# Kernel optimization log

Hardware: AMD Instinct MI355X
Metric: run time of the kernel (lower is better)

## Reference

```python
import jax, jax.numpy as jnp
import numpy as np

N, E, C = 25000, 400000, 64
NUM_ELEM, NUM_BESSEL, HID, NPATH, L = 4, 8, 64, 5, 2
R_MAX, AVG_NN = 5.0, 16.0
SQRT3, SQRT2 = 3.0 ** 0.5, 2.0 ** 0.5


def setup_inputs() -> dict:
    key = jax.random.key(0)
    ks = jax.random.split(key, 16)
    def w(k, shape, fan_in):
        return jax.random.normal(k, shape, jnp.float32) / np.float32(np.sqrt(fan_in))
    return {
        "positions": jax.random.normal(ks[0], (N, 3), jnp.float32),
        "species": jax.random.randint(ks[1], (N,), 0, NUM_ELEM, jnp.int32),
        "edge_index": jax.random.randint(ks[2], (2, E), 0, N, jnp.int32),
        "node_embed_W": w(ks[3], (NUM_ELEM, C), NUM_ELEM),
        "lin_up_W0": w(ks[4], (L, C, C), C),
        "lin_up_W1": w(ks[5], (L, C, C), C),
        "mlp_W1": w(ks[6], (L, NUM_BESSEL, HID), NUM_BESSEL),
        "mlp_W2": w(ks[7], (L, HID, HID), HID),
        "mlp_W3": w(ks[8], (L, HID, NPATH * C), HID),
        "lin_W0": w(ks[9], (L, C, C), C),
        "lin_W1": w(ks[10], (L, C, C), C),
        "prod_W0": w(ks[11], (L, NUM_ELEM, 3, C), 3),
        "prod_W1": w(ks[12], (L, NUM_ELEM, 2, C), 2),
        "prod_lin_W0": w(ks[13], (L, C, C), C),
        "prod_lin_W1": w(ks[14], (L, C, C), C),
    }


def _poly_cutoff(r):  # MACE polynomial cutoff, p=6
    p = 6.0
    x = r / R_MAX
    f = (1.0 - 0.5 * (p + 1.0) * (p + 2.0) * x ** 6
         + p * (p + 2.0) * x ** 7 - 0.5 * p * (p + 1.0) * x ** 8)
    return f * (x < 1.0)


def reference(positions, species, edge_index, node_embed_W,
              lin_up_W0, lin_up_W1, mlp_W1, mlp_W2, mlp_W3,
              lin_W0, lin_W1, prod_W0, prod_W1, prod_lin_W0, prod_lin_W1):
    sender, receiver = edge_index[0], edge_index[1]
    vec = positions[sender] - positions[receiver]                  # [E,3]
    r = jnp.maximum(jnp.linalg.norm(vec, axis=-1), 1e-6)           # [E]
    u = vec / r[:, None]
    Y1 = SQRT3 * u                                                 # l=1 SH (component norm); Y0 == 1
    # Bessel radial embedding with polynomial cutoff -> edge_feats [E, NUM_BESSEL]
    n = jnp.arange(1, NUM_BESSEL + 1, dtype=jnp.float32)
    bessel = jnp.sqrt(2.0 / R_MAX) * jnp.sin(n[None, :] * jnp.pi * r[:, None] / R_MAX) / r[:, None]
    edge_feats = bessel * _poly_cutoff(r)[:, None]
    node_attrs = jax.nn.one_hot(species, NUM_ELEM, dtype=jnp.float32)  # [N,4]
    h0 = node_attrs @ node_embed_W                                 # [N,C] scalars
    h1 = jnp.zeros((N, C, 3), jnp.float32)                         # [N,C,3] vectors
    for l in range(L):
        # linear up-projection (per-l channel mixing)
        x0 = h0 @ lin_up_W0[l]
        x1 = jnp.einsum('ncd,ck->nkd', h1, lin_up_W1[l])
        # per-edge radial MLP -> tensor-product path weights [E,5,C]
        tpw = jax.nn.silu(edge_feats @ mlp_W1[l])
        tpw = jax.nn.silu(tpw @ mlp_W2[l])
        tpw = (tpw @ mlp_W3[l]).reshape(E, NPATH, C)
        xs0, xs1 = x0[sender], x1[sender]                          # gather senders
        # CG tensor product (uvu): paths 0x0->0, 0x1->1, 1x0->1, 1x1->0, 1x1->1
        m0 = tpw[:, 0] * xs0 + tpw[:, 3] * (jnp.einsum('ecd,ed->ec', xs1, Y1) / SQRT3)
        m1 = (tpw[:, 1][..., None] * xs0[..., None] * Y1[:, None, :]
              + tpw[:, 2][..., None] * xs1
              + tpw[:, 4][..., None] * jnp.cross(xs1, Y1[:, None, :]) / SQRT2)
        # scatter-sum aggregation over receivers
        M0 = jax.ops.segment_sum(m0, receiver, num_segments=N) / AVG_NN
        M1 = jax.ops.segment_sum(m1, receiver, num_segments=N) / AVG_NN
        h0 = M0 @ lin_W0[l]
        h1 = jnp.einsum('ncd,ck->nkd', M1, lin_W1[l])
        # equivariant product basis (correlation-2 symmetric contraction, element-dependent weights)
        pw0 = jnp.einsum('ne,epc->npc', node_attrs, prod_W0[l])    # [N,3,C]
        paths0 = jnp.stack([h0, h0 * h0, (h1 * h1).sum(-1) / SQRT3], axis=1)
        b0 = (pw0 * paths0).sum(1)
        pw1 = jnp.einsum('ne,epc->npc', node_attrs, prod_W1[l])    # [N,2,C]
        b1 = pw1[:, 0][..., None] * h1 + pw1[:, 1][..., None] * (h0[..., None] * h1)
        h0 = b0 @ prod_lin_W0[l]
        h1 = jnp.einsum('ncd,ck->nkd', b1, prod_lin_W1[l])
    return jnp.concatenate([h0[..., None], h1], axis=-1)           # [N,C,4]
```

## Files before the change

kernel.cpp:

```cpp
#include <hip/hip_runtime.h>
#include <math.h>

#define CDIM 64
#define NBES 8

#define SQRT3_F     1.7320508075688772f
#define INV_SQRT3_F 0.57735026918962576f
#define INV_SQRT2_F 0.70710678118654752f
#define INV_AVG_NN  0.0625f

__device__ __forceinline__ float silu(float x) {
    return x / (1.0f + expf(-x));
}


__global__ __launch_bounds__(256) void k_hist(const int* __restrict__ eidx,
                                              int* __restrict__ cnt, int ne) {
    int e = blockIdx.x * 256 + threadIdx.x;
    if (e < ne) atomicAdd(&cnt[eidx[e]], 1);
}

__global__ __launch_bounds__(1024) void k_scan(int* __restrict__ cnt, int nn) {
    __shared__ int part[1024];
    const int t = threadIdx.x;
    const int chunk = (nn + 1023) / 1024;
    const int lo = t * chunk;
    const int hi = min(lo + chunk, nn);
    int sum = 0;
    for (int i = lo; i < hi; ++i) sum += cnt[i];
    part[t] = sum;
    __syncthreads();
    for (int off = 1; off < 1024; off <<= 1) {
        int v = (t >= off) ? part[t - off] : 0;
        __syncthreads();
        part[t] += v;
        __syncthreads();
    }
    int run = (t == 0) ? 0 : part[t - 1];
    for (int i = lo; i < hi; ++i) {
        int c = cnt[i];
        cnt[i] = run;
        run += c;
    }
}

__global__ __launch_bounds__(256) void k_scatter(const int* __restrict__ eidx,
                                                 int* __restrict__ cnt,
                                                 int* __restrict__ eidx2,
                                                 int ne) {
    int e = blockIdx.x * 256 + threadIdx.x;
    if (e < ne) {
        int s = eidx[e];
        int p = atomicAdd(&cnt[s], 1);
        eidx2[p] = s;
        eidx2[ne + p] = eidx[ne + e];
    }
}

__global__ __launch_bounds__(256) void k_lin0(
    float* __restrict__ h0, float* __restrict__ h1,
    const int* __restrict__ species, const float* __restrict__ embedW,
    const float* __restrict__ W0, float* __restrict__ x0, int nnodes) {
    const int w = threadIdx.x >> 6, k = threadIdx.x & 63;
    const int n = blockIdx.x * 4 + w;
    if (n >= nnodes) return;
    const float* er = embedW + species[n] * 64;
    float a0 = 0.f;
    for (int c = 0; c < 64; ++c) a0 = fmaf(er[c], W0[c * 64 + k], a0);
    x0[n * 64 + k] = a0;
    h0[n * 64 + k] = 0.f;
    h1[n * 192 + k] = 0.f;
    h1[n * 192 + 64 + k] = 0.f;
    h1[n * 192 + 128 + k] = 0.f;
}

__global__ __launch_bounds__(320, 4) void k_edge0(
    const float* __restrict__ pos, const int* __restrict__ eidx,
    const float* __restrict__ x0,
    const float* __restrict__ W1, const float* __restrict__ W2,
    const float* __restrict__ W3,
    float* __restrict__ M0, float* __restrict__ M1, int nedges) {
    __shared__ __align__(16) float sFEAT[64][8];
    __shared__ float sY1[64][3];
    __shared__ int sSend[64];
    __shared__ int sRecv[64];
    __shared__ __align__(16) float sH2[64 * 68];
    __shared__ __align__(16) float sU0[4352];

    float* const sH1T = sU0;
    float* const sTP = sU0;

    const int t = threadIdx.x;
    const int wv = t >> 6;

    if (t < 64) {
        int e = blockIdx.x * 64 + t;
        int s = 0, r = 0;
        float y0 = 0.f, y1 = 0.f, y2 = 0.f;
        float feats[NBES];
#pragma unroll
        for (int b = 0; b < NBES; ++b) feats[b] = 0.f;
        if (e < nedges) {
            s = eidx[e];
            r = eidx[nedges + e];
            double dx = (double)pos[3 * s + 0] - (double)pos[3 * r + 0];
            double dy = (double)pos[3 * s + 1] - (double)pos[3 * r + 1];
            double dz = (double)pos[3 * s + 2] - (double)pos[3 * r + 2];
            double rr = sqrt(dx * dx + dy * dy + dz * dz);
            if (rr < 1e-6) rr = 1e-6;
            double inv = 1.0 / rr;
            y0 = (float)(1.7320508075688772 * dx * inv);
            y1 = (float)(1.7320508075688772 * dy * inv);
            y2 = (float)(1.7320508075688772 * dz * inv);
            double xx = rr * 0.2;
            double f = 0.0;
            if (xx < 1.0) {
                double x2 = xx * xx, x3 = x2 * xx, x6 = x3 * x3;
                f = 1.0 - 28.0 * x6 + 48.0 * x6 * xx - 21.0 * x6 * x2;
            }
            double pref = 0.63245553203367587 * f * inv;
#pragma unroll
            for (int b = 0; b < NBES; ++b) {
                double arg = (double)(b + 1) * 3.14159265358979324 * rr * 0.2;
                feats[b] = (float)(sin(arg) * pref);
            }
        }
        sSend[t] = s;
        sRecv[t] = r;
        sY1[t][0] = y0; sY1[t][1] = y1; sY1[t][2] = y2;
#pragma unroll
        for (int b = 0; b < NBES; ++b) sFEAT[t][b] = feats[b];
    }
    __syncthreads();

    if (t < 256) {
        const int j = t & 63;
        float w1c[NBES];
#pragma unroll
        for (int b = 0; b < NBES; ++b) w1c[b] = W1[b * 64 + j];
#pragma unroll
        for (int i = 0; i < 16; ++i) {
            int el = wv * 16 + i;
            const float4* fr = (const float4*)(&sFEAT[el][0]);
            float4 f0 = fr[0], f1 = fr[1];
            float acc = 0.f;
            acc = fmaf(f0.x, w1c[0], acc);
            acc = fmaf(f0.y, w1c[1], acc);
            acc = fmaf(f0.z, w1c[2], acc);
            acc = fmaf(f0.w, w1c[3], acc);
            acc = fmaf(f1.x, w1c[4], acc);
            acc = fmaf(f1.y, w1c[5], acc);
            acc = fmaf(f1.z, w1c[6], acc);
            acc = fmaf(f1.w, w1c[7], acc);
            sH1T[j * 68 + el] = silu(acc);
        }
    }
    __syncthreads();

    if (t < 256) {
        const int eg = t >> 4;
        const int j4 = (t & 15) * 4;
        float a00 = 0.f, a01 = 0.f, a02 = 0.f, a03 = 0.f;
        float a10 = 0.f, a11 = 0.f, a12 = 0.f, a13 = 0.f;
        float a20 = 0.f, a21 = 0.f, a22 = 0.f, a23 = 0.f;
        float a30 = 0.f, a31 = 0.f, a32 = 0.f, a33 = 0.f;
#pragma unroll 4
        for (int k = 0; k < 64; ++k) {
            float4 av = *(const float4*)&sH1T[k * 68 + 4 * eg];
            float4 wv4 = *(const float4*)&W2[k * 64 + j4];
            a00 = fmaf(av.x, wv4.x, a00); a01 = fmaf(av.x, wv4.y, a01);
            a02 = fmaf(av.x, wv4.z, a02); a03 = fmaf(av.x, wv4.w, a03);
            a10 = fmaf(av.y, wv4.x, a10); a11 = fmaf(av.y, wv4.y, a11);
            a12 = fmaf(av.y, wv4.z, a12); a13 = fmaf(av.y, wv4.w, a13);
            a20 = fmaf(av.z, wv4.x, a20); a21 = fmaf(av.z, wv4.y, a21);
            a22 = fmaf(av.z, wv4.z, a22); a23 = fmaf(av.z, wv4.w, a23);
            a30 = fmaf(av.w, wv4.x, a30); a31 = fmaf(av.w, wv4.y, a31);
            a32 = fmaf(av.w, wv4.z, a32); a33 = fmaf(av.w, wv4.w, a33);
        }
        *(float4*)&sH2[(4 * eg + 0) * 68 + j4] =
            make_float4(silu(a00), silu(a01), silu(a02), silu(a03));
        *(float4*)&sH2[(4 * eg + 1) * 68 + j4] =
            make_float4(silu(a10), silu(a11), silu(a12), silu(a13));
        *(float4*)&sH2[(4 * eg + 2) * 68 + j4] =
            make_float4(silu(a20), silu(a21), silu(a22), silu(a23));
        *(float4*)&sH2[(4 * eg + 3) * 68 + j4] =
            make_float4(silu(a30), silu(a31), silu(a32), silu(a33));
    }
    __syncthreads();

    const int eb16 = t & 15;
    const int cb8 = (t >> 4) * 8;
    float acc[4][8];
#pragma unroll
    for (int i = 0; i < 4; ++i)
#pragma unroll
        for (int j = 0; j < 8; ++j) acc[i][j] = 0.f;

    if (t < 256) {
#pragma unroll 1
        for (int kt = 0; kt < 16; ++kt) {
            float4 h[4];
#pragma unroll
            for (int i = 0; i < 4; ++i)
                h[i] = *(const float4*)&sH2[(i * 16 + eb16) * 68 + kt * 4];
#pragma unroll
            for (int kk = 0; kk < 4; ++kk) {
                const int k = kt * 4 + kk;
                float4 wa = *(const float4*)&W3[k * 320 + cb8];
                float4 wb = *(const float4*)&W3[k * 320 + cb8 + 4];
#pragma unroll
                for (int i = 0; i < 4; ++i) {
                    float hv = (kk == 0) ? h[i].x
                             : (kk == 1) ? h[i].y
                             : (kk == 2) ? h[i].z
                                         : h[i].w;
                    acc[i][0] = fmaf(hv, wa.x, acc[i][0]);
                    acc[i][1] = fmaf(hv, wa.y, acc[i][1]);
                    acc[i][2] = fmaf(hv, wa.z, acc[i][2]);
                    acc[i][3] = fmaf(hv, wa.w, acc[i][3]);
                    acc[i][4] = fmaf(hv, wb.x, acc[i][4]);
                    acc[i][5] = fmaf(hv, wb.y, acc[i][5]);
                    acc[i][6] = fmaf(hv, wb.z, acc[i][6]);
                    acc[i][7] = fmaf(hv, wb.w, acc[i][7]);
                }
            }
        }
    }

    const int p0 = cb8 >> 6;
    const int c0 = cb8 & 63;
#pragma unroll
    for (int g = 0; g < 4; ++g) {
        if (t < 256) {
            const int row = (p0 * 16 + eb16) * 68 + c0;
            *(float4*)&sTP[row] =
                make_float4(acc[g][0], acc[g][1], acc[g][2], acc[g][3]);
            *(float4*)&sTP[row + 4] =
                make_float4(acc[g][4], acc[g][5], acc[g][6], acc[g][7]);
        }
        __syncthreads();
        for (int v = t; v < 1024; v += 320) {
            int i = v >> 6, cc = v & 63;
            int el = g * 16 + i;
            int s = sSend[el], r = sRecv[el];
            float X0 = x0[s * 64 + cc];
            float Yx = sY1[el][0], Yy = sY1[el][1], Yz = sY1[el][2];
            float t0 = sTP[(0 * 16 + i) * 68 + cc];
            float t1 = sTP[(1 * 16 + i) * 68 + cc];
            float m0 = t0 * X0;
            float m1 = t1 * X0 * INV_AVG_NN;
            atomicAdd(&M0[r * 64 + cc], m0 * INV_AVG_NN);
            atomicAdd(&M1[r * 192 + cc], m1 * Yx);
            atomicAdd(&M1[r * 192 + 64 + cc], m1 * Yy);
            atomicAdd(&M1[r * 192 + 128 + cc], m1 * Yz);
        }
        __syncthreads();
    }
}

__global__ __launch_bounds__(320, 4) void k_edge(
    const float* __restrict__ pos, const int* __restrict__ eidx,
    const float* __restrict__ x0, const float* __restrict__ x1,
    const float* __restrict__ W1, const float* __restrict__ W2,
    const float* __restrict__ W3,
    float* __restrict__ M0, float* __restrict__ M1, int nedges) {
    __shared__ __align__(16) float sFEAT[64][8];
    __shared__ float sY1[64][3];
    __shared__ int sSend[64];
    __shared__ int sRecv[64];
    __shared__ __align__(16) float sH2[64 * 68];
    __shared__ __align__(16) float sU[5440];

    float* const sH1T = sU;
    float* const sTP = sU;

    const int t = threadIdx.x;
    const int eb = t & 7;
    const int cb8 = (t >> 3) * 8;
    const int wv = t >> 6;
    const int c0 = cb8 & 63;

    if (t < 64) {
        int e = blockIdx.x * 64 + t;
        int s = 0, r = 0;
        float y0 = 0.f, y1 = 0.f, y2 = 0.f;
        float feats[NBES];
#pragma unroll
        for (int b = 0; b < NBES; ++b) feats[b] = 0.f;
        if (e < nedges) {
            s = eidx[e];
            r = eidx[nedges + e];
            double dx = (double)pos[3 * s + 0] - (double)pos[3 * r + 0];
            double dy = (double)pos[3 * s + 1] - (double)pos[3 * r + 1];
            double dz = (double)pos[3 * s + 2] - (double)pos[3 * r + 2];
            double rr = sqrt(dx * dx + dy * dy + dz * dz);
            if (rr < 1e-6) rr = 1e-6;
            double inv = 1.0 / rr;
            y0 = (float)(1.7320508075688772 * dx * inv);
            y1 = (float)(1.7320508075688772 * dy * inv);
            y2 = (float)(1.7320508075688772 * dz * inv);
            double xx = rr * 0.2;
            double f = 0.0;
            if (xx < 1.0) {
                double x2 = xx * xx, x3 = x2 * xx, x6 = x3 * x3;
                f = 1.0 - 28.0 * x6 + 48.0 * x6 * xx - 21.0 * x6 * x2;
            }
            double pref = 0.63245553203367587 * f * inv;
#pragma unroll
            for (int b = 0; b < NBES; ++b) {
                double arg = (double)(b + 1) * 3.14159265358979324 * rr * 0.2;
                feats[b] = (float)(sin(arg) * pref);
            }
        }
        sSend[t] = s;
        sRecv[t] = r;
        sY1[t][0] = y0; sY1[t][1] = y1; sY1[t][2] = y2;
#pragma unroll
        for (int b = 0; b < NBES; ++b) sFEAT[t][b] = feats[b];
    }
    __syncthreads();

    if (t < 256) {
        const int j = t & 63;
        float w1c[NBES];
#pragma unroll
        for (int b = 0; b < NBES; ++b) w1c[b] = W1[b * 64 + j];
#pragma unroll
        for (int i = 0; i < 16; ++i) {
            int el = wv * 16 + i;
            const float4* fr = (const float4*)(&sFEAT[el][0]);
            float4 f0 = fr[0], f1 = fr[1];
            float acc = 0.f;
            acc = fmaf(f0.x, w1c[0], acc);
            acc = fmaf(f0.y, w1c[1], acc);
            acc = fmaf(f0.z, w1c[2], acc);
            acc = fmaf(f0.w, w1c[3], acc);
            acc = fmaf(f1.x, w1c[4], acc);
            acc = fmaf(f1.y, w1c[5], acc);
            acc = fmaf(f1.z, w1c[6], acc);
            acc = fmaf(f1.w, w1c[7], acc);
            sH1T[j * 68 + el] = silu(acc);
        }
    }
    __syncthreads();

    if (t < 256) {
        const int eg = t >> 4;
        const int j4 = (t & 15) * 4;
        float a00 = 0.f, a01 = 0.f, a02 = 0.f, a03 = 0.f;
        float a10 = 0.f, a11 = 0.f, a12 = 0.f, a13 = 0.f;
        float a20 = 0.f, a21 = 0.f, a22 = 0.f, a23 = 0.f;
        float a30 = 0.f, a31 = 0.f, a32 = 0.f, a33 = 0.f;
#pragma unroll 4
        for (int k = 0; k < 64; ++k) {
            float4 av = *(const float4*)&sH1T[k * 68 + 4 * eg];
            float4 wv4 = *(const float4*)&W2[k * 64 + j4];
            a00 = fmaf(av.x, wv4.x, a00); a01 = fmaf(av.x, wv4.y, a01);
            a02 = fmaf(av.x, wv4.z, a02); a03 = fmaf(av.x, wv4.w, a03);
            a10 = fmaf(av.y, wv4.x, a10); a11 = fmaf(av.y, wv4.y, a11);
            a12 = fmaf(av.y, wv4.z, a12); a13 = fmaf(av.y, wv4.w, a13);
            a20 = fmaf(av.z, wv4.x, a20); a21 = fmaf(av.z, wv4.y, a21);
            a22 = fmaf(av.z, wv4.z, a22); a23 = fmaf(av.z, wv4.w, a23);
            a30 = fmaf(av.w, wv4.x, a30); a31 = fmaf(av.w, wv4.y, a31);
            a32 = fmaf(av.w, wv4.z, a32); a33 = fmaf(av.w, wv4.w, a33);
        }
        *(float4*)&sH2[(4 * eg + 0) * 68 + j4] =
            make_float4(silu(a00), silu(a01), silu(a02), silu(a03));
        *(float4*)&sH2[(4 * eg + 1) * 68 + j4] =
            make_float4(silu(a10), silu(a11), silu(a12), silu(a13));
        *(float4*)&sH2[(4 * eg + 2) * 68 + j4] =
            make_float4(silu(a20), silu(a21), silu(a22), silu(a23));
        *(float4*)&sH2[(4 * eg + 3) * 68 + j4] =
            make_float4(silu(a30), silu(a31), silu(a32), silu(a33));
    }
    __syncthreads();

    float acc[8][8];
#pragma unroll
    for (int i = 0; i < 8; ++i)
#pragma unroll
        for (int j = 0; j < 8; ++j) acc[i][j] = 0.f;

#pragma unroll 1
    for (int kt = 0; kt < 16; ++kt) {
        float4 h[8];
#pragma unroll
        for (int i = 0; i < 8; ++i)
            h[i] = *(const float4*)&sH2[(i * 8 + eb) * 68 + kt * 4];
#pragma unroll
        for (int kk = 0; kk < 4; ++kk) {
            const int k = kt * 4 + kk;
            float4 wa = *(const float4*)&W3[k * 320 + cb8];
            float4 wb = *(const float4*)&W3[k * 320 + cb8 + 4];
#pragma unroll
            for (int i = 0; i < 8; ++i) {
                float hv = (kk == 0) ? h[i].x
                         : (kk == 1) ? h[i].y
                         : (kk == 2) ? h[i].z
                                     : h[i].w;
                acc[i][0] = fmaf(hv, wa.x, acc[i][0]);
                acc[i][1] = fmaf(hv, wa.y, acc[i][1]);
                acc[i][2] = fmaf(hv, wa.z, acc[i][2]);
                acc[i][3] = fmaf(hv, wa.w, acc[i][3]);
                acc[i][4] = fmaf(hv, wb.x, acc[i][4]);
                acc[i][5] = fmaf(hv, wb.y, acc[i][5]);
                acc[i][6] = fmaf(hv, wb.z, acc[i][6]);
                acc[i][7] = fmaf(hv, wb.w, acc[i][7]);
            }
        }
    }

#pragma unroll
    for (int g = 0; g < 4; ++g) {
        {
            const int rowA = (wv * 16 + eb) * 68 + c0;
            const int rowB = (wv * 16 + 8 + eb) * 68 + c0;
            *(float4*)&sTP[rowA] =
                make_float4(acc[2 * g][0], acc[2 * g][1], acc[2 * g][2], acc[2 * g][3]);
            *(float4*)&sTP[rowA + 4] =
                make_float4(acc[2 * g][4], acc[2 * g][5], acc[2 * g][6], acc[2 * g][7]);
            *(float4*)&sTP[rowB] =
                make_float4(acc[2 * g + 1][0], acc[2 * g + 1][1], acc[2 * g + 1][2], acc[2 * g + 1][3]);
            *(float4*)&sTP[rowB + 4] =
                make_float4(acc[2 * g + 1][4], acc[2 * g + 1][5], acc[2 * g + 1][6], acc[2 * g + 1][7]);
        }
        __syncthreads();
        for (int v = t; v < 1024; v += 320) {
            int i = v >> 6, cc = v & 63;
            int el = g * 16 + i;
            int s = sSend[el], r = sRecv[el];
            float X0 = x0[s * 64 + cc];
            float Xx = x1[s * 192 + cc];
            float Xy = x1[s * 192 + 64 + cc];
            float Xz = x1[s * 192 + 128 + cc];
            float Yx = sY1[el][0], Yy = sY1[el][1], Yz = sY1[el][2];
            float t0 = sTP[(0 * 16 + i) * 68 + cc];
            float t1 = sTP[(1 * 16 + i) * 68 + cc];
            float t2 = sTP[(2 * 16 + i) * 68 + cc];
            float t3 = sTP[(3 * 16 + i) * 68 + cc];
            float t4 = sTP[(4 * 16 + i) * 68 + cc];
            float dotp = Xx * Yx + Xy * Yy + Xz * Yz;
            float m0 = t0 * X0 + t3 * (dotp * INV_SQRT3_F);
            float cx = Xy * Yz - Xz * Yy;
            float cy = Xz * Yx - Xx * Yz;
            float cz = Xx * Yy - Xy * Yx;
            float m1x = t1 * X0 * Yx + t2 * Xx + t4 * (cx * INV_SQRT2_F);
            float m1y = t1 * X0 * Yy + t2 * Xy + t4 * (cy * INV_SQRT2_F);
            float m1z = t1 * X0 * Yz + t2 * Xz + t4 * (cz * INV_SQRT2_F);
            atomicAdd(&M0[r * 64 + cc], m0 * INV_AVG_NN);
            atomicAdd(&M1[r * 192 + cc], m1x * INV_AVG_NN);
            atomicAdd(&M1[r * 192 + 64 + cc], m1y * INV_AVG_NN);
            atomicAdd(&M1[r * 192 + 128 + cc], m1z * INV_AVG_NN);
        }
        __syncthreads();
    }
}

__global__ __launch_bounds__(256) void k_nodelin(
    float* __restrict__ h0, float* __restrict__ h1,
    const int* __restrict__ species,
    const float* __restrict__ linW0, const float* __restrict__ linW1,
    const float* __restrict__ prodW0, const float* __restrict__ prodW1,
    const float* __restrict__ plinW0, const float* __restrict__ plinW1,
    const float* __restrict__ lupW0, const float* __restrict__ lupW1,
    float* __restrict__ x0, float* __restrict__ x1, int nnodes) {
    __shared__ float sh[4][4][64];
    const int w = threadIdx.x >> 6, k = threadIdx.x & 63;
    const int n = blockIdx.x * 4 + w;
    const bool valid = n < nnodes;
    float v0 = valid ? h0[n * 64 + k] : 0.f;
    float v1 = valid ? h1[n * 192 + k] : 0.f;
    float v2 = valid ? h1[n * 192 + 64 + k] : 0.f;
    float v3 = valid ? h1[n * 192 + 128 + k] : 0.f;
    sh[w][0][k] = v0; sh[w][1][k] = v1; sh[w][2][k] = v2; sh[w][3][k] = v3;
    if (valid) {
        h0[n * 64 + k] = 0.f;
        h1[n * 192 + k] = 0.f;
        h1[n * 192 + 64 + k] = 0.f;
        h1[n * 192 + 128 + k] = 0.f;
    }
    __syncthreads();
    float a0 = 0.f, a1 = 0.f, a2 = 0.f, a3 = 0.f;
    for (int c = 0; c < 64; ++c) {
        float w0 = linW0[c * 64 + k], w1 = linW1[c * 64 + k];
        a0 = fmaf(sh[w][0][c], w0, a0);
        a1 = fmaf(sh[w][1][c], w1, a1);
        a2 = fmaf(sh[w][2][c], w1, a2);
        a3 = fmaf(sh[w][3][c], w1, a3);
    }
    int sp = valid ? species[n] : 0;
    float p00 = prodW0[sp * 192 + k];
    float p01 = prodW0[sp * 192 + 64 + k];
    float p02 = prodW0[sp * 192 + 128 + k];
    float p10 = prodW1[sp * 128 + k];
    float p11 = prodW1[sp * 128 + 64 + k];
    float nsq = a1 * a1 + a2 * a2 + a3 * a3;
    float b0 = p00 * a0 + p01 * (a0 * a0) + p02 * (nsq * INV_SQRT3_F);
    float b1x = p10 * a1 + p11 * (a0 * a1);
    float b1y = p10 * a2 + p11 * (a0 * a2);
    float b1z = p10 * a3 + p11 * (a0 * a3);
    __syncthreads();
    sh[w][0][k] = b0; sh[w][1][k] = b1x; sh[w][2][k] = b1y; sh[w][3][k] = b1z;
    __syncthreads();
    a0 = a1 = a2 = a3 = 0.f;
    for (int c = 0; c < 64; ++c) {
        float w0 = plinW0[c * 64 + k], w1 = plinW1[c * 64 + k];
        a0 = fmaf(sh[w][0][c], w0, a0);
        a1 = fmaf(sh[w][1][c], w1, a1);
        a2 = fmaf(sh[w][2][c], w1, a2);
        a3 = fmaf(sh[w][3][c], w1, a3);
    }
    __syncthreads();
    sh[w][0][k] = a0; sh[w][1][k] = a1; sh[w][2][k] = a2; sh[w][3][k] = a3;
    __syncthreads();
    a0 = a1 = a2 = a3 = 0.f;
    for (int c = 0; c < 64; ++c) {
        float w0 = lupW0[c * 64 + k], w1 = lupW1[c * 64 + k];
        a0 = fmaf(sh[w][0][c], w0, a0);
        a1 = fmaf(sh[w][1][c], w1, a1);
        a2 = fmaf(sh[w][2][c], w1, a2);
        a3 = fmaf(sh[w][3][c], w1, a3);
    }
    if (valid) {
        x0[n * 64 + k] = a0;
        x1[n * 192 + k] = a1;
        x1[n * 192 + 64 + k] = a2;
        x1[n * 192 + 128 + k] = a3;
    }
}

__global__ __launch_bounds__(256) void k_nodeout(
    const float* __restrict__ h0, const float* __restrict__ h1,
    const int* __restrict__ species,
    const float* __restrict__ linW0, const float* __restrict__ linW1,
    const float* __restrict__ prodW0, const float* __restrict__ prodW1,
    const float* __restrict__ plinW0, const float* __restrict__ plinW1,
    float4* __restrict__ out, int nnodes) {
    __shared__ float sh[4][4][64];
    const int w = threadIdx.x >> 6, k = threadIdx.x & 63;
    const int n = blockIdx.x * 4 + w;
    const bool valid = n < nnodes;
    float v0 = valid ? h0[n * 64 + k] : 0.f;
    float v1 = valid ? h1[n * 192 + k] : 0.f;
    float v2 = valid ? h1[n * 192 + 64 + k] : 0.f;
    float v3 = valid ? h1[n * 192 + 128 + k] : 0.f;
    sh[w][0][k] = v0; sh[w][1][k] = v1; sh[w][2][k] = v2; sh[w][3][k] = v3;
    __syncthreads();
    float a0 = 0.f, a1 = 0.f, a2 = 0.f, a3 = 0.f;
    for (int c = 0; c < 64; ++c) {
        float w0 = linW0[c * 64 + k], w1 = linW1[c * 64 + k];
        a0 = fmaf(sh[w][0][c], w0, a0);
        a1 = fmaf(sh[w][1][c], w1, a1);
        a2 = fmaf(sh[w][2][c], w1, a2);
        a3 = fmaf(sh[w][3][c], w1, a3);
    }
    int sp = valid ? species[n] : 0;
    float p00 = prodW0[sp * 192 + k];
    float p01 = prodW0[sp * 192 + 64 + k];
    float p02 = prodW0[sp * 192 + 128 + k];
    float p10 = prodW1[sp * 128 + k];
    float p11 = prodW1[sp * 128 + 64 + k];
    float nsq = a1 * a1 + a2 * a2 + a3 * a3;
    float b0 = p00 * a0 + p01 * (a0 * a0) + p02 * (nsq * INV_SQRT3_F);
    float b1x = p10 * a1 + p11 * (a0 * a1);
    float b1y = p10 * a2 + p11 * (a0 * a2);
    float b1z = p10 * a3 + p11 * (a0 * a3);
    __syncthreads();
    sh[w][0][k] = b0; sh[w][1][k] = b1x; sh[w][2][k] = b1y; sh[w][3][k] = b1z;
    __syncthreads();
    a0 = a1 = a2 = a3 = 0.f;
    for (int c = 0; c < 64; ++c) {
        float w0 = plinW0[c * 64 + k], w1 = plinW1[c * 64 + k];
        a0 = fmaf(sh[w][0][c], w0, a0);
        a1 = fmaf(sh[w][1][c], w1, a1);
        a2 = fmaf(sh[w][2][c], w1, a2);
        a3 = fmaf(sh[w][3][c], w1, a3);
    }
    if (valid) out[n * 64 + k] = make_float4(a0, a1, a2, a3);
}

extern "C" void kernel_launch(void* const* d_in, const int* in_sizes, int n_in,
                              void* d_out, int out_size, void* d_ws,
                              size_t ws_size, hipStream_t stream) {
    const float* positions = (const float*)d_in[0];
    const int* species = (const int*)d_in[1];
    const int* eidx = (const int*)d_in[2];
    const float* embedW = (const float*)d_in[3];
    const float* linupW0 = (const float*)d_in[4];
    const float* linupW1 = (const float*)d_in[5];
    const float* mlpW1 = (const float*)d_in[6];
    const float* mlpW2 = (const float*)d_in[7];
    const float* mlpW3 = (const float*)d_in[8];
    const float* linW0 = (const float*)d_in[9];
    const float* linW1 = (const float*)d_in[10];
    const float* prodW0 = (const float*)d_in[11];
    const float* prodW1 = (const float*)d_in[12];
    const float* plinW0 = (const float*)d_in[13];
    const float* plinW1 = (const float*)d_in[14];

    const int nn = in_sizes[0] / 3;
    const int ne = in_sizes[2] / 2;

    float* h0 = (float*)d_ws;
    float* h1 = h0 + (size_t)nn * 64;
    float* x0 = h1 + (size_t)nn * 192;
    float* x1 = x0 + (size_t)nn * 64;
    int* eidx2 = (int*)(x1 + (size_t)nn * 192);

    const int gridNode = (nn + 3) / 4;
    const int gridEdge = (ne + 63) / 64;
    const int gridE256 = (ne + 255) / 256;

    const size_t needed =
        ((size_t)nn * 512) * sizeof(float) + (size_t)2 * ne * sizeof(int);
    const int* eidx_use = eidx;
    if (ws_size >= needed) {
        int* cnt = (int*)x1;
        hipMemsetAsync(cnt, 0, (size_t)nn * sizeof(int), stream);
        k_hist<<<gridE256, 256, 0, stream>>>(eidx, cnt, ne);
        k_scan<<<1, 1024, 0, stream>>>(cnt, nn);
        k_scatter<<<gridE256, 256, 0, stream>>>(eidx, cnt, eidx2, ne);
        eidx_use = eidx2;
    }

    k_lin0<<<gridNode, 256, 0, stream>>>(
        h0, h1, species, embedW, linupW0, x0, nn);
    k_edge0<<<gridEdge, 320, 0, stream>>>(
        positions, eidx_use, x0, mlpW1, mlpW2, mlpW3, h0, h1, ne);

    k_nodelin<<<gridNode, 256, 0, stream>>>(
        h0, h1, species, linW0, linW1, prodW0, prodW1, plinW0, plinW1,
        linupW0 + 4096, linupW1 + 4096, x0, x1, nn);

    k_edge<<<gridEdge, 320, 0, stream>>>(
        positions, eidx_use, x0, x1, mlpW1 + 512, mlpW2 + 4096,
        mlpW3 + 20480, h0, h1, ne);

    k_nodeout<<<gridNode, 256, 0, stream>>>(
        h0, h1, species, linW0 + 4096, linW1 + 4096,
        prodW0 + 768, prodW1 + 512, plinW0 + 4096, plinW1 + 4096,
        (float4*)d_out, nn);
}
```

Measured before the change: 1.253 ms.

## Sort edges by receiver for layer 0 and pre-reduce atomics per receiver

The edge sort now orders edges by receiver instead of sender. In the first edge kernel, each thread walks 4 consecutive edges and accumulates contributions in registers, issuing atomics only when the receiver changes. With random indices (about 16 edges per node), consecutive sorted edges often share a receiver, so this should cut the number of global atomics. The second-layer edge kernel goes back to the original unsorted edge order, which gives up sender locality for its gathers. Only 256 of 320 threads now take part in the scatter phase.

Result: faster. 1.133 ms (-9.6%).

```diff
diff --git a/kernel.cpp b/kernel.cpp
--- a/kernel.cpp
+++ b/kernel.cpp
@@ -17,7 +17,7 @@
 __global__ __launch_bounds__(256) void k_hist(const int* __restrict__ eidx,
                                               int* __restrict__ cnt, int ne) {
     int e = blockIdx.x * 256 + threadIdx.x;
-    if (e < ne) atomicAdd(&cnt[eidx[e]], 1);
+    if (e < ne) atomicAdd(&cnt[eidx[ne + e]], 1);
 }
 
 __global__ __launch_bounds__(1024) void k_scan(int* __restrict__ cnt, int nn) {
@@ -50,10 +50,10 @@
                                                  int ne) {
     int e = blockIdx.x * 256 + threadIdx.x;
     if (e < ne) {
-        int s = eidx[e];
-        int p = atomicAdd(&cnt[s], 1);
-        eidx2[p] = s;
-        eidx2[ne + p] = eidx[ne + e];
+        int r = eidx[ne + e];
+        int p = atomicAdd(&cnt[r], 1);
+        eidx2[p] = eidx[e];
+        eidx2[ne + p] = r;
     }
 }
 
@@ -239,20 +239,39 @@
                 make_float4(acc[g][4], acc[g][5], acc[g][6], acc[g][7]);
         }
         __syncthreads();
-        for (int v = t; v < 1024; v += 320) {
-            int i = v >> 6, cc = v & 63;
-            int el = g * 16 + i;
-            int s = sSend[el], r = sRecv[el];
-            float X0 = x0[s * 64 + cc];
-            float Yx = sY1[el][0], Yy = sY1[el][1], Yz = sY1[el][2];
-            float t0 = sTP[(0 * 16 + i) * 68 + cc];
-            float t1 = sTP[(1 * 16 + i) * 68 + cc];
-            float m0 = t0 * X0;
-            float m1 = t1 * X0 * INV_AVG_NN;
-            atomicAdd(&M0[r * 64 + cc], m0 * INV_AVG_NN);
-            atomicAdd(&M1[r * 192 + cc], m1 * Yx);
-            atomicAdd(&M1[r * 192 + 64 + cc], m1 * Yy);
-            atomicAdd(&M1[r * 192 + 128 + cc], m1 * Yz);
+        if (t < 256) {
+            const int q = t >> 6, cc = t & 63;
+            int r_cur = -1;
+            float a0 = 0.f, ax = 0.f, ay = 0.f, az = 0.f;
+#pragma unroll
+            for (int j = 0; j < 4; ++j) {
+                int i = q * 4 + j;
+                int el = g * 16 + i;
+                int s = sSend[el], r = sRecv[el];
+                if (r != r_cur) {
+                    if (r_cur >= 0) {
+                        atomicAdd(&M0[r_cur * 64 + cc], a0);
+                        atomicAdd(&M1[r_cur * 192 + cc], ax);
+                        atomicAdd(&M1[r_cur * 192 + 64 + cc], ay);
+                        atomicAdd(&M1[r_cur * 192 + 128 + cc], az);
+                    }
+                    r_cur = r;
+                    a0 = ax = ay = az = 0.f;
+                }
+                float X0 = x0[s * 64 + cc];
+                float t0v = sTP[(0 * 16 + i) * 68 + cc];
+                float t1v = sTP[(1 * 16 + i) * 68 + cc];
+                float m0 = t0v * X0 * INV_AVG_NN;
+                float m1 = t1v * X0 * INV_AVG_NN;
+                a0 += m0;
+                ax = fmaf(m1, sY1[el][0], ax);
+                ay = fmaf(m1, sY1[el][1], ay);
+                az = fmaf(m1, sY1[el][2], az);
+            }
+            atomicAdd(&M0[r_cur * 64 + cc], a0);
+            atomicAdd(&M1[r_cur * 192 + cc], ax);
+            atomicAdd(&M1[r_cur * 192 + 64 + cc], ay);
+            atomicAdd(&M1[r_cur * 192 + 128 + cc], az);
         }
         __syncthreads();
     }
@@ -613,27 +632,27 @@
 
     const size_t needed =
         ((size_t)nn * 512) * sizeof(float) + (size_t)2 * ne * sizeof(int);
-    const int* eidx_use = eidx;
+    const int* eidx0_use = eidx;
     if (ws_size >= needed) {
         int* cnt = (int*)x1;
         hipMemsetAsync(cnt, 0, (size_t)nn * sizeof(int), stream);
         k_hist<<<gridE256, 256, 0, stream>>>(eidx, cnt, ne);
         k_scan<<<1, 1024, 0, stream>>>(cnt, nn);
         k_scatter<<<gridE256, 256, 0, stream>>>(eidx, cnt, eidx2, ne);
-        eidx_use = eidx2;
+        eidx0_use = eidx2;
     }
 
     k_lin0<<<gridNode, 256, 0, stream>>>(
         h0, h1, species, embedW, linupW0, x0, nn);
     k_edge0<<<gridEdge, 320, 0, stream>>>(
-        positions, eidx_use, x0, mlpW1, mlpW2, mlpW3, h0, h1, ne);
+        positions, eidx0_use, x0, mlpW1, mlpW2, mlpW3, h0, h1, ne);
 
     k_nodelin<<<gridNode, 256, 0, stream>>>(
         h0, h1, species, linW0, linW1, prodW0, prodW1, plinW0, plinW1,
         linupW0 + 4096, linupW1 + 4096, x0, x1, nn);
 
     k_edge<<<gridEdge, 320, 0, stream>>>(
-        positions, eidx_use, x0, x1, mlpW1 + 512, mlpW2 + 4096,
+        positions, eidx, x0, x1, mlpW1 + 512, mlpW2 + 4096,
         mlpW3 + 20480, h0, h1, ne);
 
     k_nodeout<<<gridNode, 256, 0, stream>>>(
```
